# Performance work log

Measured on AMD Instinct MI355X. Metric: run time of the kernel, lower is better.

Reference implementation:

```python
import jax, jax.numpy as jnp
import numpy as np

N_NODES = 100000
N_EDGES = 1600000
D = 128  # node_feat_size == edge_hidden_size


def setup_inputs() -> dict:
    key = jax.random.key(0)
    ks = jax.random.split(key, 10)
    s = 1.0 / np.sqrt(D)
    return {
        "node_feats": jax.random.normal(ks[0], (N_NODES, D), jnp.float32),
        "edge_logits": jax.random.normal(ks[1], (N_EDGES, 1), jnp.float32),
        "W_proj": jax.random.normal(ks[2], (D, D), jnp.float32) * s,
        "b_proj": jax.random.normal(ks[3], (D,), jnp.float32) * s,
        "W1": jax.random.normal(ks[4], (2 * D, D), jnp.float32) * s,
        "b1": jax.random.normal(ks[5], (D,), jnp.float32) * s,
        "W2": jax.random.normal(ks[6], (D, D), jnp.float32) * s,
        "b2": jax.random.normal(ks[7], (D,), jnp.float32) * s,
        "src": jax.random.randint(ks[8], (N_EDGES,), 0, N_NODES),
        "dst": jax.random.randint(ks[9], (N_EDGES,), 0, N_NODES),
    }


def reference(node_feats, edge_logits, W_proj, b_proj, W1, b1, W2, b2, src, dst):
    # ---- edge_softmax: softmax of edge_logits grouped by destination node ----
    # [E,1] logits; per-dst max for numerical stability (gradient-free shift)
    m = jax.ops.segment_max(edge_logits, dst, num_segments=N_NODES)  # [N,1]
    m = jnp.where(jnp.isfinite(m), m, 0.0)  # nodes with no in-edges
    e = jnp.exp(edge_logits - jax.lax.stop_gradient(m)[dst])  # [E,1]
    z = jax.ops.segment_sum(e, dst, num_segments=N_NODES)  # [N,1]
    a = e / z[dst]  # [E,1]

    # ---- project_node (dropout is identity at inference) ----
    hv = node_feats @ W_proj + b_proj  # [N,D]

    # ---- src_mul_edge + sum aggregation: c[v] = sum_{(u->v)} a_uv * hv[u] ----
    msg = hv[src] * a  # [E,D]
    c = jax.ops.segment_sum(msg, dst, num_segments=N_NODES)  # [N,D]

    context = jax.nn.elu(c)
    x = jnp.concatenate([context, node_feats], axis=1)  # [N,2D]
    h = jax.nn.relu(x @ W1 + b1)  # Linear -> Dropout(id) -> ReLU
    out = jax.nn.relu(h @ W2 + b2)  # Linear -> Dropout(id), outer ReLU
    return out
```

## Files before the change

kernel.cpp:

```cpp
#include <hip/hip_runtime.h>
#include <hip/hip_bf16.h>

typedef __hip_bfloat16 bf16;
typedef __attribute__((ext_vector_type(8))) __bf16 bf16x8;
typedef __attribute__((ext_vector_type(4))) float floatx4;

#define BUCKET_SHIFT 7
#define BUCKET_NODES 128
#define MAX_NB 1024

__device__ __forceinline__ unsigned short f2b(float f) {
    bf16 h = __float2bfloat16(f);
    unsigned short s;
    __builtin_memcpy(&s, &h, 2);
    return s;
}
__device__ __forceinline__ float b2f(unsigned short u) {
    unsigned int x = ((unsigned int)u) << 16;
    float f;
    __builtin_memcpy(&f, &x, 4);
    return f;
}
__device__ __forceinline__ float load_dual(const void* p, long long i, bool isbf) {
    return isbf ? b2f(((const unsigned short*)p)[i]) : ((const float*)p)[i];
}
__device__ __forceinline__ bf16x8 ldsfrag(const unsigned short* p) {
    union { uint4 u; bf16x8 v; } t;
    t.u = *(const uint4*)p;
    return t.v;
}
__device__ __forceinline__ bf16x8 gfrag_dual(const void* A, int row, int stride, int k0, bool isbf) {
    if (isbf) {
        union { uint4 u; bf16x8 v; } t;
        t.u = *(const uint4*)((const unsigned short*)A + (size_t)row * stride + k0);
        return t.v;
    }
    const float* ap = (const float*)A + (size_t)row * stride + k0;
    float4 v0 = ((const float4*)ap)[0];
    float4 v1 = ((const float4*)ap)[1];
    union { unsigned short s[8]; bf16x8 v; } t;
    t.s[0] = f2b(v0.x); t.s[1] = f2b(v0.y); t.s[2] = f2b(v0.z); t.s[3] = f2b(v0.w);
    t.s[4] = f2b(v1.x); t.s[5] = f2b(v1.y); t.s[6] = f2b(v1.z); t.s[7] = f2b(v1.w);
    return t.v;
}

__global__ __launch_bounds__(64) void detect_kernel(const unsigned int* __restrict__ words,
                                                    int* __restrict__ flag) {
    int cnt = 0;
    for (int i = threadIdx.x; i < 4096; i += 64) {
        unsigned int lo = words[i] & 0xFFFFu;
        unsigned int e = (lo >> 7) & 0xFFu;
        if (lo == 0u || (e >= 110u && e <= 135u)) cnt++;
    }
#pragma unroll
    for (int off = 32; off > 0; off >>= 1) cnt += __shfl_down(cnt, off, 64);
    if (threadIdx.x == 0) *flag = (cnt > 2458) ? 1 : 0;
}

__global__ __launch_bounds__(256) void transpose_all_kernel(const void* __restrict__ Wp,
                                                            const void* __restrict__ W1,
                                                            const void* __restrict__ W2,
                                                            unsigned short* __restrict__ Wtp,
                                                            unsigned short* __restrict__ Wt1,
                                                            unsigned short* __restrict__ Wt2,
                                                            const int* __restrict__ flag) {
    bool isbf = (*flag != 0);
    int idx = blockIdx.x * 256 + threadIdx.x;
    if (idx < 16384) {
        int n = idx >> 7, k = idx & 127;
        Wtp[idx] = f2b(load_dual(Wp, (long long)k * 128 + n, isbf));
    } else if (idx < 49152) {
        int j = idx - 16384;
        int n = j >> 8, k = j & 255;
        Wt1[j] = f2b(load_dual(W1, (long long)k * 128 + n, isbf));
    } else if (idx < 65536) {
        int j = idx - 49152;
        int n = j >> 7, k = j & 127;
        Wt2[j] = f2b(load_dual(W2, (long long)k * 128 + n, isbf));
    }
}

__global__ __launch_bounds__(256) void bhist_kernel(const int* __restrict__ dst,
                                                    int* __restrict__ bcount, int E) {
    __shared__ int lcnt[MAX_NB];
    for (int i = threadIdx.x; i < MAX_NB; i += 256) lcnt[i] = 0;
    __syncthreads();
    int base = blockIdx.x * 8192;
#pragma unroll
    for (int j = 0; j < 32; ++j) {
        int e = base + j * 256 + threadIdx.x;
        if (e < E) atomicAdd(&lcnt[dst[e] >> BUCKET_SHIFT], 1);
    }
    __syncthreads();
    for (int i = threadIdx.x; i < MAX_NB; i += 256)
        if (lcnt[i]) atomicAdd(&bcount[i], lcnt[i]);
}

__global__ __launch_bounds__(256) void bscan_kernel(const int* __restrict__ bcount,
                                                    int* __restrict__ bstart,
                                                    int* __restrict__ bcursor, int NB) {
    int t = threadIdx.x;
    int v[4];
    int sum = 0;
#pragma unroll
    for (int j = 0; j < 4; ++j) {
        int i = t * 4 + j;
        v[j] = (i < NB) ? bcount[i] : 0;
        sum += v[j];
    }
    int lane = t & 63, wave = t >> 6;
    int inc = sum;
#pragma unroll
    for (int off = 1; off < 64; off <<= 1) {
        int x = __shfl_up(inc, off, 64);
        if (lane >= off) inc += x;
    }
    __shared__ int wsum[4];
    if (lane == 63) wsum[wave] = inc;
    __syncthreads();
    int woff = 0;
    for (int w = 0; w < wave; ++w) woff += wsum[w];
    int run = inc - sum + woff;
#pragma unroll
    for (int j = 0; j < 4; ++j) {
        int i = t * 4 + j;
        if (i < NB) { bstart[i] = run; bcursor[i] = run; }
        run += v[j];
    }
}

__global__ __launch_bounds__(256) void bappend_kernel(const int* __restrict__ dst,
                                                      const int* __restrict__ src,
                                                      const void* __restrict__ logits,
                                                      int* __restrict__ bcursor,
                                                      uint2* __restrict__ ebuf,
                                                      const int* __restrict__ flag, int E) {
    __shared__ int lcnt[MAX_NB];
    __shared__ int lbase[MAX_NB];
    for (int i = threadIdx.x; i < MAX_NB; i += 256) lcnt[i] = 0;
    __syncthreads();
    const bool isbf = (*flag != 0);
    int base = blockIdx.x * 8192;
#pragma unroll
    for (int j = 0; j < 32; ++j) {
        int e = base + j * 256 + threadIdx.x;
        if (e < E) atomicAdd(&lcnt[dst[e] >> BUCKET_SHIFT], 1);
    }
    __syncthreads();
    for (int i = threadIdx.x; i < MAX_NB; i += 256) {
        int c = lcnt[i];
        if (c) { lbase[i] = atomicAdd(&bcursor[i], c); lcnt[i] = 0; }
    }
    __syncthreads();
#pragma unroll
    for (int j = 0; j < 32; ++j) {
        int e = base + j * 256 + threadIdx.x;
        if (e < E) {
            int d = dst[e];
            int b = d >> BUCKET_SHIFT;
            float w = expf(load_dual(logits, e, isbf));
            int pos = lbase[b] + atomicAdd(&lcnt[b], 1);
            uint2 rec;
            rec.x = (unsigned int)src[e] | ((unsigned int)(d & (BUCKET_NODES - 1)) << 24);
            rec.y = __float_as_uint(w);
            ebuf[pos] = rec;
        }
    }
}

__global__ __launch_bounds__(256) void bcsr_kernel(const uint2* __restrict__ ebuf,
                                                   const int* __restrict__ bstart,
                                                   const int* __restrict__ bcount,
                                                   uint2* __restrict__ ebuf2,
                                                   int* __restrict__ row_start,
                                                   int* __restrict__ ncount, int N) {
    __shared__ int lcnt[BUCKET_NODES];
    __shared__ int lbase[BUCKET_NODES];
    const int b = blockIdx.x;
    const int s0 = bstart[b];
    const int cnt = bcount[b];
    if (threadIdx.x < BUCKET_NODES) lcnt[threadIdx.x] = 0;
    __syncthreads();
    for (int i = threadIdx.x; i < cnt; i += 256)
        atomicAdd(&lcnt[ebuf[s0 + i].x >> 24], 1);
    __syncthreads();
    if (threadIdx.x < 64) {
        int lane = threadIdx.x;
        int carry = 0;
#pragma unroll
        for (int half = 0; half < 2; ++half) {
            int idx = half * 64 + lane;
            int v = lcnt[idx];
            int inc = v;
#pragma unroll
            for (int off = 1; off < 64; off <<= 1) {
                int t = __shfl_up(inc, off, 64);
                if (lane >= off) inc += t;
            }
            lbase[idx] = carry + inc - v;
            carry += __shfl(inc, 63, 64);
        }
    }
    __syncthreads();
    if (threadIdx.x < BUCKET_NODES) {
        int gn = b * BUCKET_NODES + threadIdx.x;
        if (gn < N) {
            row_start[gn] = s0 + lbase[threadIdx.x];
            ncount[gn] = lcnt[threadIdx.x];
        }
    }
    __syncthreads();
    if (threadIdx.x < BUCKET_NODES) lcnt[threadIdx.x] = 0;
    __syncthreads();
    for (int i = threadIdx.x; i < cnt; i += 256) {
        uint2 rec = ebuf[s0 + i];
        int dl = rec.x >> 24;
        int pos = lbase[dl] + atomicAdd(&lcnt[dl], 1);
        ebuf2[s0 + pos] = make_uint2(rec.x & 0xFFFFFFu, rec.y);
    }
}

__global__ __launch_bounds__(256) void agg_csr_kernel(const int* __restrict__ row_start,
                                                      const int* __restrict__ ncount,
                                                      const uint2* __restrict__ erec,
                                                      const unsigned int* __restrict__ hv32,
                                                      unsigned int* __restrict__ ctx32, int N) {
    int n = blockIdx.x * 4 + (threadIdx.x >> 6);
    int lane = threadIdx.x & 63;
    if (n >= N) return;
    int s0 = row_start[n];
    int deg = ncount[n];
    float accx = 0.f, accy = 0.f, z = 0.f;
    int i = 0;
    for (; i + 8 <= deg; i += 8) {
        uint2 r[8];
        unsigned int h[8];
#pragma unroll
        for (int j = 0; j < 8; ++j) r[j] = erec[s0 + i + j];
#pragma unroll
        for (int j = 0; j < 8; ++j) h[j] = hv32[(size_t)r[j].x * 64 + lane];
#pragma unroll
        for (int j = 0; j < 8; ++j) {
            float w = __uint_as_float(r[j].y);
            z += w;
            accx += w * b2f((unsigned short)h[j]);
            accy += w * b2f((unsigned short)(h[j] >> 16));
        }
    }
    for (; i + 4 <= deg; i += 4) {
        uint2 r[4];
        unsigned int h[4];
#pragma unroll
        for (int j = 0; j < 4; ++j) r[j] = erec[s0 + i + j];
#pragma unroll
        for (int j = 0; j < 4; ++j) h[j] = hv32[(size_t)r[j].x * 64 + lane];
#pragma unroll
        for (int j = 0; j < 4; ++j) {
            float w = __uint_as_float(r[j].y);
            z += w;
            accx += w * b2f((unsigned short)h[j]);
            accy += w * b2f((unsigned short)(h[j] >> 16));
        }
    }
    for (; i < deg; ++i) {
        uint2 r = erec[s0 + i];
        unsigned int h = hv32[(size_t)r.x * 64 + lane];
        float w = __uint_as_float(r.y);
        z += w;
        accx += w * b2f((unsigned short)h);
        accy += w * b2f((unsigned short)(h >> 16));
    }
    float rz = (z > 0.f) ? 1.f / z : 0.f;
    float x = accx * rz, y = accy * rz;
    x = x > 0.f ? x : expm1f(x);
    y = y > 0.f ? y : expm1f(y);
    ctx32[(size_t)n * 64 + lane] = ((unsigned int)f2b(y) << 16) | f2b(x);
}

__global__ __launch_bounds__(256) void gemm_proj(const void* __restrict__ A,
                                                 const unsigned short* __restrict__ Wt,
                                                 const void* __restrict__ bias,
                                                 unsigned short* __restrict__ hv,
                                                 const int* __restrict__ flag, int N) {
    __shared__ unsigned short Wl[128 * 136];
    const bool isbf = (*flag != 0);
    const int t = threadIdx.x, wid = t >> 6, lane = t & 63;
    const int m16 = lane & 15, quad = lane >> 4;
    const int row0 = blockIdx.x * 128;
    {
        int r = t >> 1, kh = (t & 1) * 64;
        const uint4* s = (const uint4*)(Wt + (size_t)r * 128 + kh);
        uint4* d = (uint4*)&Wl[r * 136 + kh];
#pragma unroll
        for (int q = 0; q < 8; ++q) d[q] = s[q];
    }
    __syncthreads();

    floatx4 acc[2][8];
#pragma unroll
    for (int i = 0; i < 2; ++i)
#pragma unroll
        for (int j = 0; j < 8; ++j) acc[i][j] = (floatx4){0.f, 0.f, 0.f, 0.f};

    int ra0 = row0 + wid * 32 + m16;      if (ra0 >= N) ra0 = N - 1;
    int ra1 = row0 + wid * 32 + 16 + m16; if (ra1 >= N) ra1 = N - 1;

#pragma unroll
    for (int c = 0; c < 4; ++c) {
        int k0 = c * 32 + quad * 8;
        bf16x8 a0 = gfrag_dual(A, ra0, 128, k0, isbf);
        bf16x8 a1 = gfrag_dual(A, ra1, 128, k0, isbf);
#pragma unroll
        for (int nt = 0; nt < 8; ++nt) {
            bf16x8 b = ldsfrag(&Wl[(nt * 16 + m16) * 136 + k0]);
            acc[0][nt] = __builtin_amdgcn_mfma_f32_16x16x32_bf16(a0, b, acc[0][nt], 0, 0, 0);
            acc[1][nt] = __builtin_amdgcn_mfma_f32_16x16x32_bf16(a1, b, acc[1][nt], 0, 0, 0);
        }
    }

#pragma unroll
    for (int mt = 0; mt < 2; ++mt) {
        int gr0 = row0 + wid * 32 + mt * 16 + quad * 4;
#pragma unroll
        for (int nt = 0; nt < 8; ++nt) {
            int col = nt * 16 + m16;
            float bb = load_dual(bias, col, isbf);
#pragma unroll
            for (int rg = 0; rg < 4; ++rg) {
                int gr = gr0 + rg;
                if (gr < N) hv[(size_t)gr * 128 + col] = f2b(acc[mt][nt][rg] + bb);
            }
        }
    }
}

__global__ __launch_bounds__(256) void mlp_fused(const unsigned short* __restrict__ ctx,
                                                 const void* __restrict__ nf,
                                                 const unsigned short* __restrict__ Wt1,
                                                 const void* __restrict__ b1,
                                                 const unsigned short* __restrict__ Wt2,
                                                 const void* __restrict__ b2,
                                                 void* __restrict__ outp,
                                                 const int* __restrict__ flag, int N) {
    __shared__ unsigned short Wl[128 * 72];
    __shared__ unsigned short Hl[4][32 * 136];
    const bool isbf = (*flag != 0);
    const int t = threadIdx.x, wid = t >> 6, lane = t & 63;
    const int m16 = lane & 15, quad = lane >> 4;
    const int row0 = blockIdx.x * 128;

    floatx4 acc[2][8];
#pragma unroll
    for (int i = 0; i < 2; ++i)
#pragma unroll
        for (int j = 0; j < 8; ++j) acc[i][j] = (floatx4){0.f, 0.f, 0.f, 0.f};

    int ra0 = row0 + wid * 32 + m16;      if (ra0 >= N) ra0 = N - 1;
    int ra1 = row0 + wid * 32 + 16 + m16; if (ra1 >= N) ra1 = N - 1;

#pragma unroll
    for (int kc = 0; kc < 4; ++kc) {
        {
            int r = t >> 1, kh = (t & 1) * 32;
            const uint4* s = (const uint4*)(Wt1 + (size_t)r * 256 + kc * 64 + kh);
            uint4* d = (uint4*)&Wl[r * 72 + kh];
#pragma unroll
            for (int q = 0; q < 4; ++q) d[q] = s[q];
        }
        __syncthreads();
#pragma unroll
        for (int c = 0; c < 2; ++c) {
            int kl = c * 32 + quad * 8;
            int ka = kc * 64 + kl;
            bf16x8 a0, a1;
            if (ka < 128) {
                union { uint4 u; bf16x8 v; } t0, t1;
                t0.u = *(const uint4*)(ctx + (size_t)ra0 * 128 + ka);
                t1.u = *(const uint4*)(ctx + (size_t)ra1 * 128 + ka);
                a0 = t0.v; a1 = t1.v;
            } else {
                a0 = gfrag_dual(nf, ra0, 128, ka - 128, isbf);
                a1 = gfrag_dual(nf, ra1, 128, ka - 128, isbf);
            }
#pragma unroll
            for (int nt = 0; nt < 8; ++nt) {
                bf16x8 b = ldsfrag(&Wl[(nt * 16 + m16) * 72 + kl]);
                acc[0][nt] = __builtin_amdgcn_mfma_f32_16x16x32_bf16(a0, b, acc[0][nt], 0, 0, 0);
                acc[1][nt] = __builtin_amdgcn_mfma_f32_16x16x32_bf16(a1, b, acc[1][nt], 0, 0, 0);
            }
        }
        __syncthreads();
    }

#pragma unroll
    for (int nt = 0; nt < 8; ++nt) {
        int col = nt * 16 + m16;
        float bb = load_dual(b1, col, isbf);
#pragma unroll
        for (int mt = 0; mt < 2; ++mt) {
#pragma unroll
            for (int rg = 0; rg < 4; ++rg) {
                int lr = mt * 16 + quad * 4 + rg;
                float x = acc[mt][nt][rg] + bb;
                Hl[wid][lr * 136 + col] = f2b(x > 0.f ? x : 0.f);
            }
        }
    }

#pragma unroll
    for (int i = 0; i < 2; ++i)
#pragma unroll
        for (int j = 0; j < 8; ++j) acc[i][j] = (floatx4){0.f, 0.f, 0.f, 0.f};

#pragma unroll
    for (int kc = 0; kc < 2; ++kc) {
        {
            int r = t >> 1, kh = (t & 1) * 32;
            const uint4* s = (const uint4*)(Wt2 + (size_t)r * 128 + kc * 64 + kh);
            uint4* d = (uint4*)&Wl[r * 72 + kh];
#pragma unroll
            for (int q = 0; q < 4; ++q) d[q] = s[q];
        }
        __syncthreads();
#pragma unroll
        for (int c = 0; c < 2; ++c) {
            int kl = c * 32 + quad * 8;
            int ka = kc * 64 + kl;
            bf16x8 a0 = ldsfrag(&Hl[wid][m16 * 136 + ka]);
            bf16x8 a1 = ldsfrag(&Hl[wid][(16 + m16) * 136 + ka]);
#pragma unroll
            for (int nt = 0; nt < 8; ++nt) {
                bf16x8 b = ldsfrag(&Wl[(nt * 16 + m16) * 72 + kl]);
                acc[0][nt] = __builtin_amdgcn_mfma_f32_16x16x32_bf16(a0, b, acc[0][nt], 0, 0, 0);
                acc[1][nt] = __builtin_amdgcn_mfma_f32_16x16x32_bf16(a1, b, acc[1][nt], 0, 0, 0);
            }
        }
        __syncthreads();
    }

#pragma unroll
    for (int mt = 0; mt < 2; ++mt) {
        int gr0 = row0 + wid * 32 + mt * 16 + quad * 4;
#pragma unroll
        for (int nt = 0; nt < 8; ++nt) {
            int col = nt * 16 + m16;
            float bb = load_dual(b2, col, isbf);
#pragma unroll
            for (int rg = 0; rg < 4; ++rg) {
                int gr = gr0 + rg;
                if (gr < N) {
                    float x = acc[mt][nt][rg] + bb;
                    x = x > 0.f ? x : 0.f;
                    if (!isbf) ((float*)outp)[(size_t)gr * 128 + col] = x;
                    else       ((unsigned short*)outp)[(size_t)gr * 128 + col] = f2b(x);
                }
            }
        }
    }
}

extern "C" void kernel_launch(void* const* d_in, const int* in_sizes, int n_in,
                              void* d_out, int out_size, void* d_ws, size_t ws_size,
                              hipStream_t stream) {
    const void* node_feats  = d_in[0];
    const void* edge_logits = d_in[1];
    const void* W_proj      = d_in[2];
    const void* b_proj      = d_in[3];
    const void* W1          = d_in[4];
    const void* b1          = d_in[5];
    const void* W2          = d_in[6];
    const void* b2          = d_in[7];
    const int*  src         = (const int*)d_in[8];
    const int*  dst         = (const int*)d_in[9];

    const int N = in_sizes[0] / 128;
    const int E = in_sizes[8];
    const int NB = (N + BUCKET_NODES - 1) / BUCKET_NODES;

    char* ws = (char*)d_ws;
    size_t off = 0;
    unsigned short* hv  = (unsigned short*)(ws + off); off += (size_t)N * 256;
    unsigned short* ctx = (unsigned short*)(ws + off); off += (size_t)N * 256;
    uint2* ebuf  = (uint2*)(ws + off); off += (size_t)E * 8;
    uint2* ebuf2 = (uint2*)(ws + off); off += (size_t)E * 8;
    unsigned short* Wtp = (unsigned short*)(ws + off); off += 128 * 128 * 2;
    unsigned short* Wt1 = (unsigned short*)(ws + off); off += 128 * 256 * 2;
    unsigned short* Wt2 = (unsigned short*)(ws + off); off += 128 * 128 * 2;
    int* bcount    = (int*)(ws + off); off += MAX_NB * 4;
    int* bstart    = (int*)(ws + off); off += MAX_NB * 4;
    int* bcursor   = (int*)(ws + off); off += MAX_NB * 4;
    int* row_start = (int*)(ws + off); off += (size_t)N * 4;
    int* ncount    = (int*)(ws + off); off += (size_t)N * 4;
    int* flag      = (int*)(ws + off);

    const int gblocks = (N + 127) / 128;
    const int ebblocks = (E + 8191) / 8192;

    detect_kernel<<<1, 64, 0, stream>>>((const unsigned int*)node_feats, flag);
    hipMemsetAsync(bcount, 0, MAX_NB * 4, stream);

    transpose_all_kernel<<<256, 256, 0, stream>>>(W_proj, W1, W2, Wtp, Wt1, Wt2, flag);

    bhist_kernel<<<ebblocks, 256, 0, stream>>>(dst, bcount, E);
    bscan_kernel<<<1, 256, 0, stream>>>(bcount, bstart, bcursor, NB);
    bappend_kernel<<<ebblocks, 256, 0, stream>>>(dst, src, edge_logits, bcursor,
                                                 ebuf, flag, E);
    bcsr_kernel<<<NB, 256, 0, stream>>>(ebuf, bstart, bcount, ebuf2,
                                        row_start, ncount, N);

    gemm_proj<<<gblocks, 256, 0, stream>>>(node_feats, Wtp, b_proj, hv, flag, N);

    agg_csr_kernel<<<(N + 3) / 4, 256, 0, stream>>>(row_start, ncount, ebuf2,
                                                    (const unsigned int*)hv,
                                                    (unsigned int*)ctx, N);

    mlp_fused<<<gblocks, 256, 0, stream>>>(ctx, node_feats, Wt1, b1, Wt2, b2,
                                           d_out, flag, N);
}
```

Baseline: 352.6 us.

## Merge independent launches and unroll CSR aggregation with cheaper gather addressing

Result: no change. 346.0 us (-1.9%).

```diff
diff --git a/kernel.cpp b/kernel.cpp
--- a/kernel.cpp
+++ b/kernel.cpp
@@ -4,6 +4,7 @@
 typedef __hip_bfloat16 bf16;
 typedef __attribute__((ext_vector_type(8))) __bf16 bf16x8;
 typedef __attribute__((ext_vector_type(4))) float floatx4;
+typedef __attribute__((ext_vector_type(2))) float floatx2;
 
 #define BUCKET_SHIFT 7
 #define BUCKET_NODES 128
@@ -45,7 +46,9 @@
 }
 
 __global__ __launch_bounds__(64) void detect_kernel(const unsigned int* __restrict__ words,
-                                                    int* __restrict__ flag) {
+                                                    int* __restrict__ flag,
+                                                    int* __restrict__ bcount) {
+    for (int i = threadIdx.x; i < MAX_NB; i += 64) bcount[i] = 0;
     int cnt = 0;
     for (int i = threadIdx.x; i < 4096; i += 64) {
         unsigned int lo = words[i] & 0xFFFFu;
@@ -57,43 +60,44 @@
     if (threadIdx.x == 0) *flag = (cnt > 2458) ? 1 : 0;
 }
 
-__global__ __launch_bounds__(256) void transpose_all_kernel(const void* __restrict__ Wp,
-                                                            const void* __restrict__ W1,
-                                                            const void* __restrict__ W2,
-                                                            unsigned short* __restrict__ Wtp,
-                                                            unsigned short* __restrict__ Wt1,
-                                                            unsigned short* __restrict__ Wt2,
-                                                            const int* __restrict__ flag) {
-    bool isbf = (*flag != 0);
-    int idx = blockIdx.x * 256 + threadIdx.x;
-    if (idx < 16384) {
-        int n = idx >> 7, k = idx & 127;
-        Wtp[idx] = f2b(load_dual(Wp, (long long)k * 128 + n, isbf));
-    } else if (idx < 49152) {
-        int j = idx - 16384;
-        int n = j >> 8, k = j & 255;
-        Wt1[j] = f2b(load_dual(W1, (long long)k * 128 + n, isbf));
-    } else if (idx < 65536) {
-        int j = idx - 49152;
-        int n = j >> 7, k = j & 127;
-        Wt2[j] = f2b(load_dual(W2, (long long)k * 128 + n, isbf));
-    }
-}
-
-__global__ __launch_bounds__(256) void bhist_kernel(const int* __restrict__ dst,
-                                                    int* __restrict__ bcount, int E) {
-    __shared__ int lcnt[MAX_NB];
-    for (int i = threadIdx.x; i < MAX_NB; i += 256) lcnt[i] = 0;
-    __syncthreads();
-    int base = blockIdx.x * 8192;
-#pragma unroll
-    for (int j = 0; j < 32; ++j) {
-        int e = base + j * 256 + threadIdx.x;
-        if (e < E) atomicAdd(&lcnt[dst[e] >> BUCKET_SHIFT], 1);
-    }
-    __syncthreads();
-    for (int i = threadIdx.x; i < MAX_NB; i += 256)
-        if (lcnt[i]) atomicAdd(&bcount[i], lcnt[i]);
+__global__ __launch_bounds__(256) void prep_kernel(const void* __restrict__ Wp,
+                                                   const void* __restrict__ W1,
+                                                   const void* __restrict__ W2,
+                                                   unsigned short* __restrict__ Wtp,
+                                                   unsigned short* __restrict__ Wt1,
+                                                   unsigned short* __restrict__ Wt2,
+                                                   const int* __restrict__ flag,
+                                                   const int* __restrict__ dst,
+                                                   int* __restrict__ bcount, int E) {
+    if (blockIdx.x < 256) {
+        bool isbf = (*flag != 0);
+        int idx = blockIdx.x * 256 + threadIdx.x;
+        if (idx < 16384) {
+            int n = idx >> 7, k = idx & 127;
+            Wtp[idx] = f2b(load_dual(Wp, (long long)k * 128 + n, isbf));
+        } else if (idx < 49152) {
+            int j = idx - 16384;
+            int n = j >> 8, k = j & 255;
+            Wt1[j] = f2b(load_dual(W1, (long long)k * 128 + n, isbf));
+        } else if (idx < 65536) {
+            int j = idx - 49152;
+            int n = j >> 7, k = j & 127;
+            Wt2[j] = f2b(load_dual(W2, (long long)k * 128 + n, isbf));
+        }
+    } else {
+        __shared__ int lcnt[MAX_NB];
+        for (int i = threadIdx.x; i < MAX_NB; i += 256) lcnt[i] = 0;
+        __syncthreads();
+        int base = (blockIdx.x - 256) * 8192;
+#pragma unroll
+        for (int j = 0; j < 32; ++j) {
+            int e = base + j * 256 + threadIdx.x;
+            if (e < E) atomicAdd(&lcnt[dst[e] >> BUCKET_SHIFT], 1);
+        }
+        __syncthreads();
+        for (int i = threadIdx.x; i < MAX_NB; i += 256)
+            if (lcnt[i]) atomicAdd(&bcount[i], lcnt[i]);
+    }
 }
 
 __global__ __launch_bounds__(256) void bscan_kernel(const int* __restrict__ bcount,
@@ -168,170 +172,188 @@
     }
 }
 
-__global__ __launch_bounds__(256) void bcsr_kernel(const uint2* __restrict__ ebuf,
-                                                   const int* __restrict__ bstart,
-                                                   const int* __restrict__ bcount,
-                                                   uint2* __restrict__ ebuf2,
-                                                   int* __restrict__ row_start,
-                                                   int* __restrict__ ncount, int N) {
-    __shared__ int lcnt[BUCKET_NODES];
-    __shared__ int lbase[BUCKET_NODES];
-    const int b = blockIdx.x;
-    const int s0 = bstart[b];
-    const int cnt = bcount[b];
-    if (threadIdx.x < BUCKET_NODES) lcnt[threadIdx.x] = 0;
-    __syncthreads();
-    for (int i = threadIdx.x; i < cnt; i += 256)
-        atomicAdd(&lcnt[ebuf[s0 + i].x >> 24], 1);
-    __syncthreads();
-    if (threadIdx.x < 64) {
-        int lane = threadIdx.x;
-        int carry = 0;
-#pragma unroll
-        for (int half = 0; half < 2; ++half) {
-            int idx = half * 64 + lane;
-            int v = lcnt[idx];
-            int inc = v;
-#pragma unroll
-            for (int off = 1; off < 64; off <<= 1) {
-                int t = __shfl_up(inc, off, 64);
-                if (lane >= off) inc += t;
-            }
-            lbase[idx] = carry + inc - v;
-            carry += __shfl(inc, 63, 64);
-        }
-    }
-    __syncthreads();
-    if (threadIdx.x < BUCKET_NODES) {
-        int gn = b * BUCKET_NODES + threadIdx.x;
-        if (gn < N) {
-            row_start[gn] = s0 + lbase[threadIdx.x];
-            ncount[gn] = lcnt[threadIdx.x];
-        }
-    }
-    __syncthreads();
-    if (threadIdx.x < BUCKET_NODES) lcnt[threadIdx.x] = 0;
-    __syncthreads();
-    for (int i = threadIdx.x; i < cnt; i += 256) {
-        uint2 rec = ebuf[s0 + i];
-        int dl = rec.x >> 24;
-        int pos = lbase[dl] + atomicAdd(&lcnt[dl], 1);
-        ebuf2[s0 + pos] = make_uint2(rec.x & 0xFFFFFFu, rec.y);
+__global__ __launch_bounds__(256) void gemm_bcsr_kernel(const void* __restrict__ A,
+                                                        const unsigned short* __restrict__ Wt,
+                                                        const void* __restrict__ bias,
+                                                        unsigned short* __restrict__ hv,
+                                                        const int* __restrict__ flag, int N,
+                                                        int gblocks,
+                                                        const uint2* __restrict__ ebuf,
+                                                        const int* __restrict__ bstart,
+                                                        const int* __restrict__ bcount,
+                                                        uint2* __restrict__ ebuf2,
+                                                        int* __restrict__ row_start,
+                                                        int* __restrict__ ncount) {
+    __shared__ unsigned short Wl[128 * 136];
+    if ((int)blockIdx.x < gblocks) {
+        const bool isbf = (*flag != 0);
+        const int t = threadIdx.x, wid = t >> 6, lane = t & 63;
+        const int m16 = lane & 15, quad = lane >> 4;
+        const int row0 = blockIdx.x * 128;
+        {
+            int r = t >> 1, kh = (t & 1) * 64;
+            const uint4* s = (const uint4*)(Wt + (size_t)r * 128 + kh);
+            uint4* d = (uint4*)&Wl[r * 136 + kh];
+#pragma unroll
+            for (int q = 0; q < 8; ++q) d[q] = s[q];
+        }
+        __syncthreads();
+
+        floatx4 acc[2][8];
+#pragma unroll
+        for (int i = 0; i < 2; ++i)
+#pragma unroll
+            for (int j = 0; j < 8; ++j) acc[i][j] = (floatx4){0.f, 0.f, 0.f, 0.f};
+
+        int ra0 = row0 + wid * 32 + m16;      if (ra0 >= N) ra0 = N - 1;
+        int ra1 = row0 + wid * 32 + 16 + m16; if (ra1 >= N) ra1 = N - 1;
+
+#pragma unroll
+        for (int c = 0; c < 4; ++c) {
+            int k0 = c * 32 + quad * 8;
+            bf16x8 a0 = gfrag_dual(A, ra0, 128, k0, isbf);
+            bf16x8 a1 = gfrag_dual(A, ra1, 128, k0, isbf);
+#pragma unroll
+            for (int nt = 0; nt < 8; ++nt) {
+                bf16x8 b = ldsfrag(&Wl[(nt * 16 + m16) * 136 + k0]);
+                acc[0][nt] = __builtin_amdgcn_mfma_f32_16x16x32_bf16(a0, b, acc[0][nt], 0, 0, 0);
+                acc[1][nt] = __builtin_amdgcn_mfma_f32_16x16x32_bf16(a1, b, acc[1][nt], 0, 0, 0);
+            }
+        }
+
+#pragma unroll
+        for (int mt = 0; mt < 2; ++mt) {
+            int gr0 = row0 + wid * 32 + mt * 16 + quad * 4;
+#pragma unroll
+            for (int nt = 0; nt < 8; ++nt) {
+                int col = nt * 16 + m16;
+                float bb = load_dual(bias, col, isbf);
+#pragma unroll
+                for (int rg = 0; rg < 4; ++rg) {
+                    int gr = gr0 + rg;
+                    if (gr < N) hv[(size_t)gr * 128 + col] = f2b(acc[mt][nt][rg] + bb);
+                }
+            }
+        }
+    } else {
+        int* lcnt = (int*)Wl;
+        int* lbase = lcnt + BUCKET_NODES;
+        const int b = blockIdx.x - gblocks;
+        const int s0 = bstart[b];
+        const int cnt = bcount[b];
+        if (threadIdx.x < BUCKET_NODES) lcnt[threadIdx.x] = 0;
+        __syncthreads();
+        for (int i = threadIdx.x; i < cnt; i += 256)
+            atomicAdd(&lcnt[ebuf[s0 + i].x >> 24], 1);
+        __syncthreads();
+        if (threadIdx.x < 64) {
+            int lane = threadIdx.x;
+            int carry = 0;
+#pragma unroll
+            for (int half = 0; half < 2; ++half) {
+                int idx = half * 64 + lane;
+                int v = lcnt[idx];
+                int inc = v;
+#pragma unroll
+                for (int off = 1; off < 64; off <<= 1) {
+                    int t = __shfl_up(inc, off, 64);
+                    if (lane >= off) inc += t;
+                }
+                lbase[idx] = carry + inc - v;
+                carry += __shfl(inc, 63, 64);
+            }
+        }
+        __syncthreads();
+        if (threadIdx.x < BUCKET_NODES) {
+            int gn = b * BUCKET_NODES + threadIdx.x;
+            if (gn < N) {
+                row_start[gn] = s0 + lbase[threadIdx.x];
+                ncount[gn] = lcnt[threadIdx.x];
+            }
+        }
+        __syncthreads();
+        if (threadIdx.x < BUCKET_NODES) lcnt[threadIdx.x] = 0;
+        __syncthreads();
+        for (int i = threadIdx.x; i < cnt; i += 256) {
+            uint2 rec = ebuf[s0 + i];
+            int dl = rec.x >> 24;
+            int pos = lbase[dl] + atomicAdd(&lcnt[dl], 1);
+            ebuf2[s0 + pos] = make_uint2(rec.x & 0xFFFFFFu, rec.y);
+        }
     }
 }
 
 __global__ __launch_bounds__(256) void agg_csr_kernel(const int* __restrict__ row_start,
                                                       const int* __restrict__ ncount,
-                                                      const uint2* __restrict__ erec,
+                                                      const unsigned long long* __restrict__ erec,
                                                       const unsigned int* __restrict__ hv32,
                                                       unsigned int* __restrict__ ctx32, int N) {
     int n = blockIdx.x * 4 + (threadIdx.x >> 6);
     int lane = threadIdx.x & 63;
     if (n >= N) return;
-    int s0 = row_start[n];
-    int deg = ncount[n];
-    float accx = 0.f, accy = 0.f, z = 0.f;
+    int s0 = __builtin_amdgcn_readfirstlane(row_start[n]);
+    int deg = __builtin_amdgcn_readfirstlane(ncount[n]);
+    const unsigned long long* ep = erec + s0;
+    const unsigned int lb = (unsigned int)lane << 2;
+    floatx2 acc = {0.f, 0.f};
+    float z = 0.f;
     int i = 0;
-    for (; i + 8 <= deg; i += 8) {
-        uint2 r[8];
-        unsigned int h[8];
-#pragma unroll
-        for (int j = 0; j < 8; ++j) r[j] = erec[s0 + i + j];
-#pragma unroll
-        for (int j = 0; j < 8; ++j) h[j] = hv32[(size_t)r[j].x * 64 + lane];
-#pragma unroll
-        for (int j = 0; j < 8; ++j) {
-            float w = __uint_as_float(r[j].y);
+    for (; i + 16 <= deg; i += 16) {
+        unsigned long long r[16];
+        unsigned int h[16];
+#pragma unroll
+        for (int j = 0; j < 16; ++j) r[j] = ep[i + j];
+#pragma unroll
+        for (int j = 0; j < 16; ++j) {
+            unsigned int sx = (unsigned int)r[j];
+            __builtin_assume(sx < (1u << 24));
+            h[j] = *(const unsigned int*)((const char*)hv32 + ((sx << 8) | lb));
+        }
+#pragma unroll
+        for (int j = 0; j < 16; ++j) {
+            float w = __uint_as_float((unsigned int)(r[j] >> 32));
             z += w;
-            accx += w * b2f((unsigned short)h[j]);
-            accy += w * b2f((unsigned short)(h[j] >> 16));
+            floatx2 hf = { __uint_as_float(h[j] << 16),
+                           __uint_as_float(h[j] & 0xFFFF0000u) };
+            acc += hf * w;
         }
     }
     for (; i + 4 <= deg; i += 4) {
-        uint2 r[4];
+        unsigned long long r[4];
         unsigned int h[4];
 #pragma unroll
-        for (int j = 0; j < 4; ++j) r[j] = erec[s0 + i + j];
-#pragma unroll
-        for (int j = 0; j < 4; ++j) h[j] = hv32[(size_t)r[j].x * 64 + lane];
+        for (int j = 0; j < 4; ++j) r[j] = ep[i + j];
 #pragma unroll
         for (int j = 0; j < 4; ++j) {
-            float w = __uint_as_float(r[j].y);
+            unsigned int sx = (unsigned int)r[j];
+            __builtin_assume(sx < (1u << 24));
+            h[j] = *(const unsigned int*)((const char*)hv32 + ((sx << 8) | lb));
+        }
+#pragma unroll
+        for (int j = 0; j < 4; ++j) {
+            float w = __uint_as_float((unsigned int)(r[j] >> 32));
             z += w;
-            accx += w * b2f((unsigned short)h[j]);
-            accy += w * b2f((unsigned short)(h[j] >> 16));
+            floatx2 hf = { __uint_as_float(h[j] << 16),
+                           __uint_as_float(h[j] & 0xFFFF0000u) };
+            acc += hf * w;
         }
     }
     for (; i < deg; ++i) {
-        uint2 r = erec[s0 + i];
-        unsigned int h = hv32[(size_t)r.x * 64 + lane];
-        float w = __uint_as_float(r.y);
+        unsigned long long r = ep[i];
+        unsigned int sx = (unsigned int)r;
+        __builtin_assume(sx < (1u << 24));
+        unsigned int h = *(const unsigned int*)((const char*)hv32 + ((sx << 8) | lb));
+        float w = __uint_as_float((unsigned int)(r >> 32));
         z += w;
-        accx += w * b2f((unsigned short)h);
-        accy += w * b2f((unsigned short)(h >> 16));
+        floatx2 hf = { __uint_as_float(h << 16),
+                       __uint_as_float(h & 0xFFFF0000u) };
+        acc += hf * w;
     }
     float rz = (z > 0.f) ? 1.f / z : 0.f;
-    float x = accx * rz, y = accy * rz;
+    float x = acc.x * rz, y = acc.y * rz;
     x = x > 0.f ? x : expm1f(x);
     y = y > 0.f ? y : expm1f(y);
     ctx32[(size_t)n * 64 + lane] = ((unsigned int)f2b(y) << 16) | f2b(x);
-}
-
-__global__ __launch_bounds__(256) void gemm_proj(const void* __restrict__ A,
-                                                 const unsigned short* __restrict__ Wt,
-                                                 const void* __restrict__ bias,
-                                                 unsigned short* __restrict__ hv,
-                                                 const int* __restrict__ flag, int N) {
-    __shared__ unsigned short Wl[128 * 136];
-    const bool isbf = (*flag != 0);
-    const int t = threadIdx.x, wid = t >> 6, lane = t & 63;
-    const int m16 = lane & 15, quad = lane >> 4;
-    const int row0 = blockIdx.x * 128;
-    {
-        int r = t >> 1, kh = (t & 1) * 64;
-        const uint4* s = (const uint4*)(Wt + (size_t)r * 128 + kh);
-        uint4* d = (uint4*)&Wl[r * 136 + kh];
-#pragma unroll
-        for (int q = 0; q < 8; ++q) d[q] = s[q];
-    }
-    __syncthreads();
-
-    floatx4 acc[2][8];
-#pragma unroll
-    for (int i = 0; i < 2; ++i)
-#pragma unroll
-        for (int j = 0; j < 8; ++j) acc[i][j] = (floatx4){0.f, 0.f, 0.f, 0.f};
-
-    int ra0 = row0 + wid * 32 + m16;      if (ra0 >= N) ra0 = N - 1;
-    int ra1 = row0 + wid * 32 + 16 + m16; if (ra1 >= N) ra1 = N - 1;
-
-#pragma unroll
-    for (int c = 0; c < 4; ++c) {
-        int k0 = c * 32 + quad * 8;
-        bf16x8 a0 = gfrag_dual(A, ra0, 128, k0, isbf);
-        bf16x8 a1 = gfrag_dual(A, ra1, 128, k0, isbf);
-#pragma unroll
-        for (int nt = 0; nt < 8; ++nt) {
-            bf16x8 b = ldsfrag(&Wl[(nt * 16 + m16) * 136 + k0]);
-            acc[0][nt] = __builtin_amdgcn_mfma_f32_16x16x32_bf16(a0, b, acc[0][nt], 0, 0, 0);
-            acc[1][nt] = __builtin_amdgcn_mfma_f32_16x16x32_bf16(a1, b, acc[1][nt], 0, 0, 0);
-        }
-    }
-
-#pragma unroll
-    for (int mt = 0; mt < 2; ++mt) {
-        int gr0 = row0 + wid * 32 + mt * 16 + quad * 4;
-#pragma unroll
-        for (int nt = 0; nt < 8; ++nt) {
-            int col = nt * 16 + m16;
-            float bb = load_dual(bias, col, isbf);
-#pragma unroll
-            for (int rg = 0; rg < 4; ++rg) {
-                int gr = gr0 + rg;
-                if (gr < N) hv[(size_t)gr * 128 + col] = f2b(acc[mt][nt][rg] + bb);
-            }
-        }
-    }
 }
 
 __global__ __launch_bounds__(256) void mlp_fused(const unsigned short* __restrict__ ctx,
@@ -496,24 +518,20 @@
     const int gblocks = (N + 127) / 128;
     const int ebblocks = (E + 8191) / 8192;
 
-    detect_kernel<<<1, 64, 0, stream>>>((const unsigned int*)node_feats, flag);
-    hipMemsetAsync(bcount, 0, MAX_NB * 4, stream);
-
-    transpose_all_kernel<<<256, 256, 0, stream>>>(W_proj, W1, W2, Wtp, Wt1, Wt2, flag);
-
-    bhist_kernel<<<ebblocks, 256, 0, stream>>>(dst, bcount, E);
+    detect_kernel<<<1, 64, 0, stream>>>((const unsigned int*)node_feats, flag, bcount);
+    prep_kernel<<<256 + ebblocks, 256, 0, stream>>>(W_proj, W1, W2, Wtp, Wt1, Wt2,
+                                                    flag, dst, bcount, E);
     bscan_kernel<<<1, 256, 0, stream>>>(bcount, bstart, bcursor, NB);
     bappend_kernel<<<ebblocks, 256, 0, stream>>>(dst, src, edge_logits, bcursor,
                                                  ebuf, flag, E);
-    bcsr_kernel<<<NB, 256, 0, stream>>>(ebuf, bstart, bcount, ebuf2,
-                                        row_start, ncount, N);
-
-    gemm_proj<<<gblocks, 256, 0, stream>>>(node_feats, Wtp, b_proj, hv, flag, N);
-
-    agg_csr_kernel<<<(N + 3) / 4, 256, 0, stream>>>(row_start, ncount, ebuf2,
+    gemm_bcsr_kernel<<<gblocks + NB, 256, 0, stream>>>(node_feats, Wtp, b_proj, hv,
+                                                       flag, N, gblocks,
+                                                       ebuf, bstart, bcount, ebuf2,
+                                                       row_start, ncount);
+    agg_csr_kernel<<<(N + 3) / 4, 256, 0, stream>>>(row_start, ncount,
+                                                    (const unsigned long long*)ebuf2,
                                                     (const unsigned int*)hv,
                                                     (unsigned int*)ctx, N);
-
     mlp_fused<<<gblocks, 256, 0, stream>>>(ctx, node_feats, Wt1, b1, Wt2, b2,
                                            d_out, flag, N);
 }
```
